# Performance work log

Hardware: AMD Instinct MI355X
Metric: run time of the kernel (lower is better)

## Reference

```python
import jax, jax.numpy as jnp
from jax import lax
import numpy as np

EPS = 1e-7          # BCE clamp
SMOOTH = 1.0        # Dice smoothing
INT_INF = jnp.int32(2**31 - 1)


def _bce_dice(p, t):
    """BCE + Dice loss (standard BCEDiceLoss): p, t float32 in [0,1]."""
    pc = jnp.clip(p, EPS, 1.0 - EPS)
    bce = -jnp.mean(t * jnp.log(pc) + (1.0 - t) * jnp.log1p(-pc))
    inter = jnp.sum(p * t)
    dice = 1.0 - (2.0 * inter + SMOOTH) / (jnp.sum(p) + jnp.sum(t) + SMOOTH)
    return bce + dice


def _ccl(mask):
    """4-connected component labeling per batch image.
    mask: [B,H,W] bool. Returns (labels, init_labels) int32; 0 = background.
    Iterative min-label propagation to a fixpoint (lax.while_loop)."""
    B, H, W = mask.shape
    init = jnp.where(mask, jnp.arange(1, B * H * W + 1, dtype=jnp.int32).reshape(B, H, W), 0)

    def step(lab):
        big = jnp.where(mask, lab, INT_INF)
        pad_h = jnp.full((B, 1, W), INT_INF, jnp.int32)
        pad_w = jnp.full((B, H, 1), INT_INF, jnp.int32)
        up    = jnp.concatenate([big[:, 1:, :], pad_h], axis=1)
        down  = jnp.concatenate([pad_h, big[:, :-1, :]], axis=1)
        left  = jnp.concatenate([big[:, :, 1:], pad_w], axis=2)
        right = jnp.concatenate([pad_w, big[:, :, :-1]], axis=2)
        m = jnp.minimum(big, jnp.minimum(jnp.minimum(up, down), jnp.minimum(left, right)))
        return jnp.where(mask, m, 0)

    def cond(c):
        return c[1]

    def body(c):
        new = step(c[0])
        return (new, jnp.any(new != c[0]))

    lab, _ = lax.while_loop(cond, body, (init, jnp.array(True)))
    return lab, init


def _forward(pred_out, target_mask, num_target_classes):
    f32 = jnp.float32
    B, C, H, W = pred_out.shape
    pred_masks = jnp.argmax(pred_out, axis=1)      # [B,H,W] int
    tm = target_mask[:, 0]                         # [B,H,W] int

    # background-vs-background BCEDice term
    res = _bce_dice((pred_masks == 0).astype(f32), (tm == 0).astype(f32))

    ph = jnp.zeros((B, H, W), f32)    # pred_placeholder
    pho = jnp.zeros((B, H, W), f32)   # pred_placeholder_out
    last_i = jnp.int32(1)

    # fixed loop over predicted classes (torch loops over unique values;
    # here: loop 1..C-1 gated by presence so absent classes are no-ops)
    for v in range(1, C):
        cur = pred_masks == v                       # class-v mask
        present = jnp.any(cur)
        lab, init = _ccl(cur)
        # number of connected components = pixels that kept their seed label
        n_comp = jnp.sum((lab == init) & cur).astype(jnp.int32)
        has_bg = jnp.any(~cur).astype(jnp.int32)    # 0 in cur_uniq?
        # sum_c (c_mask + last_i) over components == cur + n_comp*last_i everywhere
        inc = cur.astype(f32) + (n_comp * last_i).astype(f32)
        ph = jnp.where(present, ph + inc, ph)
        pho = jnp.where(cur, pred_out[:, v], pho)
        last_i = last_i + jnp.where(present, n_comp + has_bg, 0)

    # loop over nonzero target ids (bounded by num_target_classes), gated by presence
    for t in range(1, num_target_classes):
        target_m = tm == t
        present = jnp.any(target_m)
        n = jnp.sum(target_m)
        # torch.median(ph[target_m]): lower median of masked values
        vals = jnp.where(target_m.reshape(-1), ph.reshape(-1), jnp.inf)
        med = jnp.sort(vals)[jnp.maximum((n - 1) // 2, 0)]
        tm_f = target_m.astype(f32)
        contrib = _bce_dice(pho * (ph == med).astype(f32), tm_f)
        extra = jnp.sum(pho * ((ph != med) & target_m).astype(f32)) / jnp.maximum(n, 1).astype(f32)
        res = res + jnp.where(present, contrib + extra, 0.0)

    # len(torch.unique(target_mask)) with values in [0, num_target_classes)
    n_unique = jnp.sum(jnp.stack([jnp.any(tm == t) for t in range(num_target_classes)]).astype(jnp.int32))
    return res / (2 * n_unique + 1).astype(f32)


def setup_inputs() -> dict:
    key = jax.random.key(0)
    k1, k2 = jax.random.split(key)
    B, C, H, W = 8, 5, 768, 768
    pred_out = jax.random.uniform(k1, (B, C, H, W), dtype=jnp.float32)
    target_mask = jax.random.randint(k2, (B, 1, H, W), 0, 4, dtype=jnp.int32)
    return {"pred_out": pred_out, "target_mask": target_mask, "num_target_classes": 4}


def reference(pred_out, target_mask, num_target_classes):
    return _forward(pred_out, target_mask, num_target_classes)
```

## Files before the change

### kernel.cpp

```cpp
#include <hip/hip_runtime.h>
#include <stdint.h>
#include <math.h>

#define B_ 8
#define C_ 5
#define H_ 768
#define W_ 768
#define HW_ (H_*W_)
#define HWq (HW_/4)
#define NPIX (B_*HW_)
#define NQUAD (NPIX/4)
#define TB 8
#define INVAL 0xFFFFFFFFu
#define LN2F 0.69314718056f
#define BIASF 16.2f
#define TILE 64
#define TPR 12
#define TPC 12
#define NTILES (B_*TPR*TPC)
#define NNODES (NTILES*256)
#define SEAMS_PER_IMG (11*768)
#define NB_HALF (B_*SEAMS_PER_IMG)
#define NB_TOT (2*NB_HALF)
#define SEAMBLK (NB_TOT/256)
#define SBLK 2304
#define NTH (SBLK*256)

typedef unsigned long long ull;

static __device__ __forceinline__ unsigned pload(const unsigned* P, unsigned i) {
  return __hip_atomic_load(&P[i], __ATOMIC_RELAXED, __HIP_MEMORY_SCOPE_AGENT);
}
static __device__ unsigned findRootG(unsigned* P, unsigned i) {
  unsigned p = pload(P, i);
  if (p == i) return i;
  unsigned gp = pload(P, p);
  while (p != gp) {
    __hip_atomic_store(&P[i], gp, __ATOMIC_RELAXED, __HIP_MEMORY_SCOPE_AGENT);
    i = p; p = gp; gp = pload(P, p);
  }
  return p;
}
static __device__ bool uniteG(unsigned* P, unsigned a, unsigned b) {
  a = findRootG(P, a);
  b = findRootG(P, b);
  while (a != b) {
    if (a < b) { unsigned t = a; a = b; b = t; }
    unsigned old = atomicCAS(&P[a], a, b);
    if (old == a) return true;
    a = findRootG(P, old);
    b = findRootG(P, b);
  }
  return false;
}
static __device__ __forceinline__ unsigned ploadL(const unsigned* P, unsigned i) {
  return __hip_atomic_load(&P[i], __ATOMIC_RELAXED, __HIP_MEMORY_SCOPE_WORKGROUP);
}
static __device__ unsigned findRootL(const unsigned* P, unsigned i) {
  unsigned p = ploadL(P, i) & 0xFFFFu;
  while (p != i) { i = p; p = ploadL(P, i) & 0xFFFFu; }
  return i;
}
static __device__ void uniteL(unsigned* P, unsigned a, unsigned b) {
  a = findRootL(P, a);
  b = findRootL(P, b);
  while (a != b) {
    if (a < b) { unsigned t = a; a = b; b = t; }
    unsigned old = atomicCAS(&P[a], 0xFFFF0000u | a, 0xFFFF0000u | b);
    if (old == (0xFFFF0000u | a)) return;
    a = findRootL(P, old & 0xFFFFu);
    b = findRootL(P, b);
  }
}

__global__ __launch_bounds__(256) void k_stats(
    const float4* __restrict__ pred4, const int4* __restrict__ tgt4,
    unsigned* __restrict__ cls4, double* __restrict__ sp)
{
  __shared__ ull h[32][41];
  for (int i = threadIdx.x; i < 32*41; i += 256) (&h[0][0])[i] = 0ull;
  __syncthreads();
  const int cp = threadIdx.x & 31;
  const int tid = blockIdx.x * 256 + threadIdx.x;

#define DOQUAD(P0, P1, P2, P3, P4, T4, PACKED)                                 \
  {                                                                            \
    PACKED = 0u;                                                               \
    _Pragma("unroll")                                                          \
    for (int j = 0; j < 4; ++j) {                                              \
      float v0 = ((const float*)&(P0))[j];                                     \
      float v1 = ((const float*)&(P1))[j];                                     \
      float v2 = ((const float*)&(P2))[j];                                     \
      float v3 = ((const float*)&(P3))[j];                                     \
      float v4 = ((const float*)&(P4))[j];                                     \
      int tt = ((const int*)&(T4))[j];                                         \
      float best = v0; int bc = 0;                                             \
      if (v1 > best) { best = v1; bc = 1; }                                    \
      if (v2 > best) { best = v2; bc = 2; }                                    \
      if (v3 > best) { best = v3; bc = 3; }                                    \
      if (v4 > best) { best = v4; bc = 4; }                                    \
      unsigned tu = (unsigned)tt; if (tu >= TB) tu = TB - 1;                   \
      ull w;                                                                   \
      if (bc) {                                                                \
        float pc = fminf(fmaxf(best, 1e-7f), 1.0f - 1e-7f);                    \
        float l2p = __log2f(pc);                                               \
        float l2m = __log2f(1.0f - pc);                                        \
        float logit = (l2p - l2m) * LN2F;                                      \
        float mag   = -l2m * LN2F;                                             \
        w = (1ull << 57)                                                       \
          | ((ull)__float2uint_rn(best * 4096.0f) << 38)                       \
          | ((ull)__float2uint_rn((logit + BIASF) * 64.0f) << 20)              \
          | (ull)__float2uint_rn(mag * 64.0f);                                 \
      } else {                                                                 \
        w = 1ull << 57;                                                        \
      }                                                                        \
      atomicAdd(&h[cp][(int)tu * C_ + bc], w);                                 \
      PACKED |= ((unsigned)bc) << (8 * j);                                     \
    }                                                                          \
  }

  {
    int q0 = tid;
    int q1 = tid + NTH;
    int b0 = q0 / HWq, h0 = q0 - b0 * HWq;
    int b1 = q1 / HWq, h1 = q1 - b1 * HWq;
    const float4* ba = pred4 + (size_t)b0 * (C_*HWq) + h0;
    const float4* bb = pred4 + (size_t)b1 * (C_*HWq) + h1;
    float4 a0 = ba[0], a1 = ba[HWq], a2 = ba[2*HWq], a3 = ba[3*HWq], a4 = ba[4*HWq];
    float4 c0 = bb[0], c1 = bb[HWq], c2 = bb[2*HWq], c3 = bb[3*HWq], c4 = bb[4*HWq];
    int4 ta = tgt4[q0];
    int4 tb = tgt4[q1];
    unsigned pk0, pk1;
    DOQUAD(a0, a1, a2, a3, a4, ta, pk0)
    DOQUAD(c0, c1, c2, c3, c4, tb, pk1)
    cls4[q0] = pk0;
    cls4[q1] = pk1;
  }
#undef DOQUAD
  __syncthreads();
  if (threadIdx.x < 160) {
    int slot = threadIdx.x >> 2, comp = threadIdx.x & 3;
    double s = 0.0;
#pragma unroll
    for (int c = 0; c < 32; ++c) {
      ull w = h[c][slot];
      if (comp == 0)      s += (double)(w >> 57);
      else if (comp == 1) s += (double)((w >> 38) & 0x7FFFFull) * (1.0/4096.0);
      else if (comp == 2) s += (double)((w >> 20) & 0x3FFFFull) * (1.0/64.0);
      else                s += (double)(w & 0x1FFFFull) * (1.0/64.0);
    }
    sp[(size_t)blockIdx.x * 160 + threadIdx.x] = s;
  }
}

__global__ __launch_bounds__(256) void k_ccl(
    const unsigned* __restrict__ cls4, unsigned short* __restrict__ border,
    unsigned* __restrict__ P2, unsigned* __restrict__ rootcnt)
{
  __shared__ unsigned lab[TILE*TILE];
  __shared__ unsigned lclsw[TILE*TILE/4];
  __shared__ unsigned s_rt[4];
  unsigned char* lcls = (unsigned char*)lclsw;

  int blk = blockIdx.x;
  int b = blk / (TPR*TPC);
  int rem = blk - b * (TPR*TPC);
  int ty0 = (rem / TPR) * TILE;
  int tx0 = (rem - (rem / TPR) * TPR) * TILE;

  if (threadIdx.x < 4) s_rt[threadIdx.x] = 0u;
  {
    unsigned n = (unsigned)blk * 256u + threadIdx.x;
    P2[n] = n;
  }
  const int r = threadIdx.x >> 2, cq = threadIdx.x & 3;
  const int seg = r * 64 + cq * 16;
  union { uint4 q; unsigned char bch[16]; unsigned w[4]; } A, D;
  {
    const uint4* src = (const uint4*)(cls4 + ((b * HW_ + (ty0 + r) * W_ + tx0) >> 2));
    A.q = src[cq];
    *(uint4*)&lclsw[r * 16 + cq * 4] = A.q;
  }
#pragma unroll
  for (int m = 0; m < 4; ++m) {
    uint4 lw;
    unsigned* lp = (unsigned*)&lw;
#pragma unroll
    for (int k = 0; k < 4; ++k) {
      int li = seg + m * 4 + k;
      unsigned c = (A.w[m] >> (8 * k)) & 255u;
      lp[k] = c ? (0xFFFF0000u | (unsigned)li) : INVAL;
    }
    *(uint4*)&lab[seg + m * 4] = lw;
  }
  __syncthreads();

  bool hasDown = (r < 63);
  if (hasDown) D.q = *(const uint4*)&lclsw[(r + 1) * 16 + cq * 4];
  else D.q = make_uint4(0, 0, 0, 0);
  unsigned rb = (cq < 3) ? (unsigned)lcls[seg + 16] : 0u;
#pragma unroll
  for (int j = 0; j < 16; ++j) {
    unsigned c = A.bch[j];
    if (!c) continue;
    int li = seg + j;
    unsigned cr = (j < 15) ? (unsigned)A.bch[j + 1] : rb;
    if (cr == c) uniteL(lab, li, li + 1);
    if (D.bch[j] == c) uniteL(lab, li, li + 64);
  }
  __syncthreads();

#pragma unroll
  for (int m = 0; m < 4; ++m) {
    uint4 lw = *(const uint4*)&lab[seg + m * 4];
    const unsigned* lp = (const unsigned*)&lw;
#pragma unroll
    for (int k = 0; k < 4; ++k) {
      int li = seg + m * 4 + k;
      unsigned c = A.bch[m * 4 + k];
      if (c && (lp[k] & 0xFFFFu) == (unsigned)li) atomicAdd(&s_rt[c - 1], 1u);
    }
  }
  int bp = threadIdx.x;
  int tx, ty;
  if (bp < 64)       { ty = 0;  tx = bp; }
  else if (bp < 128) { ty = 63; tx = bp - 64; }
  else if (bp < 192) { tx = 0;  ty = bp - 128; }
  else               { tx = 63; ty = bp - 192; }
  int li = ty * 64 + tx;
  unsigned char c = lcls[li];
  unsigned rt = 0;
  if (c) {
    rt = findRootL(lab, (unsigned)li);
    atomicMin(&lab[rt], ((unsigned)bp << 16) | rt);
  }
  __syncthreads();
  unsigned sub = c ? (lab[rt] >> 16) : 0u;
  border[blk * 256 + bp] = (unsigned short)(((unsigned)c << 8) | sub);
  if (threadIdx.x < 4) rootcnt[blk * 4 + threadIdx.x] = s_rt[threadIdx.x];
}

__global__ __launch_bounds__(256) void k_seam(const unsigned short* __restrict__ border,
                                              unsigned* __restrict__ P2,
                                              unsigned* __restrict__ smcnt,
                                              const double* __restrict__ sp,
                                              double* __restrict__ spf)
{
  __shared__ unsigned s_sub[4];
  __shared__ double red[256];
  if (threadIdx.x < 4) s_sub[threadIdx.x] = 0u;
  __syncthreads();
  int idx = blockIdx.x * blockDim.x + threadIdx.x;
  if (idx < NB_TOT) {
    int tA, tB, pA, pB;
    if (idx < NB_HALF) {
      int b = idx / SEAMS_PER_IMG;
      int r = idx - b * SEAMS_PER_IMG;
      int seam = r / W_;
      int x = r - seam * W_;
      int tj = x >> 6, k = x & 63;
      tA = (b * TPC + seam) * TPR + tj;
      tB = tA + TPR;
      pA = tA * 256 + 64 + k;
      pB = tB * 256 + 0 + k;
    } else {
      int i2 = idx - NB_HALF;
      int b = i2 / SEAMS_PER_IMG;
      int r = i2 - b * SEAMS_PER_IMG;
      int seam = r / H_;
      int y = r - seam * H_;
      int ti = y >> 6, k = y & 63;
      tA = (b * TPC + ti) * TPR + seam;
      tB = tA + 1;
      pA = tA * 256 + 192 + k;
      pB = tB * 256 + 128 + k;
    }
    unsigned a16 = border[pA];
    unsigned b16 = border[pB];
    unsigned ca = a16 >> 8, cb = b16 >> 8;
    if (ca && ca == cb) {
      if (uniteG(P2, (unsigned)tA * 256u + (a16 & 255u),
                     (unsigned)tB * 256u + (b16 & 255u)))
        atomicAdd(&s_sub[ca - 1], 1u);
    }
  }
  __syncthreads();
  if (threadIdx.x < 4) smcnt[blockIdx.x * 4 + threadIdx.x] = s_sub[threadIdx.x];
  if (blockIdx.x < 160) {
    double s = 0.0;
    for (int j = threadIdx.x; j < SBLK; j += 256) s += sp[(size_t)j * 160 + blockIdx.x];
    red[threadIdx.x] = s;
    __syncthreads();
    for (int off = 128; off; off >>= 1) {
      if (threadIdx.x < off) red[threadIdx.x] += red[threadIdx.x + off];
      __syncthreads();
    }
    if (threadIdx.x == 0) spf[blockIdx.x] = red[0];
  }
}

#define SH_CNT(t,c)   shist[((t)*C_+(c))*4 + 0]
#define SH_PRED(t,c)  shist[((t)*C_+(c))*4 + 1]
#define SH_LRAW(t,c)  shist[((t)*C_+(c))*4 + 2]
#define SH_MAG(t,c)   shist[((t)*C_+(c))*4 + 3]
__global__ __launch_bounds__(256) void k_final(
    const double* __restrict__ spf, const unsigned* __restrict__ rootcnt,
    const unsigned* __restrict__ smcnt, const int* __restrict__ ntcp,
    float* __restrict__ out)
{
  __shared__ double shist[160];
  __shared__ double s_col[C_][3];
  __shared__ unsigned s_cnti[TB*C_];
  __shared__ unsigned s_ctot[C_];
  __shared__ unsigned s_nc[4], s_sm[4];
  __shared__ float s_ph[C_];
  __shared__ double s_term[TB];
  __shared__ int s_NT;
  __shared__ int s_nun;

  if (threadIdx.x < 4) { s_nc[threadIdx.x] = 0u; s_sm[threadIdx.x] = 0u; }
  if (threadIdx.x < TB) s_term[threadIdx.x] = 0.0;
  __syncthreads();
  if (threadIdx.x < 160) shist[threadIdx.x] = spf[threadIdx.x];
  {
    unsigned a = 0;
    for (int j = threadIdx.x; j < NTILES * 4; j += 256) a += rootcnt[j];
    if (a) atomicAdd(&s_nc[threadIdx.x & 3], a);
  }
  {
    unsigned a = 0;
    for (int j = threadIdx.x; j < SEAMBLK * 4; j += 256) a += smcnt[j];
    if (a) atomicAdd(&s_sm[threadIdx.x & 3], a);
  }
  if (threadIdx.x == 0) {
    int NT = ntcp[0];
    if (NT < 1) NT = 1;
    if (NT > TB) NT = TB;
    s_NT = NT;
  }
  __syncthreads();

  if (threadIdx.x < TB * C_) s_cnti[threadIdx.x] = (unsigned)llrint(shist[threadIdx.x * 4]);
  __syncthreads();

  if (threadIdx.x < C_) {
    int c = threadIdx.x;
    double sc = 0.0, sp2 = 0.0, sl = 0.0;
    unsigned ct = 0;
#pragma unroll
    for (int t = 0; t < TB; ++t) {
      sc += SH_CNT(t, c);
      sp2 += SH_PRED(t, c);
      sl += -SH_MAG(t, c);
      ct += s_cnti[t * C_ + c];
    }
    s_col[c][0] = sc; s_col[c][1] = sp2; s_col[c][2] = sl;
    s_ctot[c] = ct;
  }
  __syncthreads();

  if (threadIdx.x == 0) {
#pragma unroll
    for (int cc = 0; cc < C_; ++cc) {
      float ph = 0.0f;
      int li = 1;
#pragma unroll
      for (int v = 1; v < C_; ++v) {
        unsigned ncv = s_nc[v - 1] - s_sm[v - 1];
        if (s_ctot[v] > 0) {
          int prod = (int)(ncv * (unsigned)li);
          float sv = (float)prod;
          float inc = ((cc == v) ? 1.0f : 0.0f) + sv;
          ph = ph + inc;
          li = li + (int)ncv + ((s_ctot[v] < (unsigned)NPIX) ? 1 : 0);
        }
      }
      s_ph[cc] = ph;
    }
  }
  __syncthreads();

  const float EPSF = 1e-7f;
  const double L1 = (double)logf(1.0f - EPSF);
  const double M1 = (double)log1pf(-(1.0f - EPSF));
  const double L0 = (double)logf(EPSF);
  const double M0 = (double)log1pf(-EPSF);
  const double N = (double)NPIX;
  const double BIASD = (double)BIASF;
  const int NT = s_NT;

  if (threadIdx.x == 0) {
    double nt0 = 0;
#pragma unroll
    for (int c = 0; c < C_; ++c) nt0 += SH_CNT(0, c);
    double np1 = (double)s_ctot[0];
    double n11 = SH_CNT(0, 0);
    s_term[0] = -(n11*L1 + (nt0 - n11)*L0 + (np1 - n11)*M1 + (N - nt0 - np1 + n11)*M0) / N
                + 1.0 - (2.0*n11 + 1.0) / (np1 + nt0 + 1.0);
    int nun = 0;
    for (int t = 0; t < NT; ++t) {
      long long s = 0;
#pragma unroll
      for (int c = 0; c < C_; ++c) s += (long long)s_cnti[t * C_ + c];
      if (s) nun++;
    }
    s_nun = nun;
  } else if (threadIdx.x < (unsigned)NT) {
    int t = threadIdx.x;
    long long ntti = 0;
#pragma unroll
    for (int c = 0; c < C_; ++c) ntti += (long long)s_cnti[t * C_ + c];
    if (ntti != 0) {
      double ntt = 0;
#pragma unroll
      for (int c = 0; c < C_; ++c) ntt += SH_CNT(t, c);
      float ph0 = s_ph[0], ph1 = s_ph[1], ph2 = s_ph[2], ph3 = s_ph[3], ph4 = s_ph[4];
      float pht[C_] = {ph0, ph1, ph2, ph3, ph4};
      int idx[C_] = {0, 1, 2, 3, 4};
#pragma unroll
      for (int i = 1; i < C_; ++i)
        for (int j = i; j > 0 && pht[idx[j]] < pht[idx[j-1]]; --j) {
          int tmp = idx[j]; idx[j] = idx[j-1]; idx[j-1] = tmp;
        }
      long long k = (ntti - 1) / 2;
      float med = pht[idx[C_ - 1]];
      long long cum = 0;
#pragma unroll
      for (int i = 0; i < C_; ++i) {
        cum += (long long)s_cnti[t * C_ + idx[i]];
        if (cum > k) { med = pht[idx[i]]; break; }
      }
      double A = 0, Bt = 0, inter = 0, sum_p = 0, ex = 0, nfg_t = 0, nfg_all = 0;
#pragma unroll
      for (int c = 1; c < C_; ++c) {
        double cnt_tc = SH_CNT(t, c);
        double mag_tc = SH_MAG(t, c);
        double spred_tc = SH_PRED(t, c);
        if (pht[c] == med) {
          double logit = SH_LRAW(t, c) - BIASD * cnt_tc;
          A += logit - mag_tc;
          inter += spred_tc;
          nfg_t += cnt_tc;
          nfg_all += s_col[c][0];
          sum_p += s_col[c][1];
          Bt += s_col[c][2] - (-mag_tc);
        } else {
          ex += spred_tc;
        }
      }
      double bce  = -(A + Bt + (ntt - nfg_t)*L0 + (N - ntt - (nfg_all - nfg_t))*M0) / N;
      double dice = 1.0 - (2.0*inter + 1.0) / (sum_p + ntt + 1.0);
      s_term[t] = bce + dice + ex / ntt;
    }
  }
  __syncthreads();
  if (threadIdx.x == 0) {
    double res = 0.0;
#pragma unroll
    for (int t = 0; t < TB; ++t) res += s_term[t];
    out[0] = (float)(res / (double)(2 * s_nun + 1));
  }
}

extern "C" void kernel_launch(void* const* d_in, const int* in_sizes, int n_in,
                              void* d_out, int out_size, void* d_ws, size_t ws_size,
                              hipStream_t stream) {
  const float* pred = (const float*)d_in[0];
  const int* tgt = (const int*)d_in[1];
  const int* ntc = (const int*)d_in[2];
  float* out = (float*)d_out;
  char* ws = (char*)d_ws;
  size_t off = 0;
  unsigned* cls4 = (unsigned*)(ws + off);        off += (size_t)NQUAD * 4;
  double* sp = (double*)(ws + off);              off += (size_t)SBLK * 160 * 8;
  double* spf = (double*)(ws + off);             off += 160 * 8;
  unsigned* P2 = (unsigned*)(ws + off);          off += (size_t)NNODES * 4;
  unsigned short* border = (unsigned short*)(ws + off); off += (size_t)NTILES * 256 * 2;
  unsigned* rootcnt = (unsigned*)(ws + off);     off += (size_t)NTILES * 4 * 4;
  unsigned* smcnt = (unsigned*)(ws + off);       off += (size_t)SEAMBLK * 4 * 4;

  hipLaunchKernelGGL(k_stats, dim3(SBLK), dim3(256), 0, stream,
                     (const float4*)pred, (const int4*)tgt, cls4, sp);
  hipLaunchKernelGGL(k_ccl, dim3(NTILES), dim3(256), 0, stream,
                     cls4, border, P2, rootcnt);
  hipLaunchKernelGGL(k_seam, dim3(SEAMBLK), dim3(256), 0, stream,
                     border, P2, smcnt, sp, spf);
  hipLaunchKernelGGL(k_final, dim3(1), dim3(256), 0, stream,
                     spf, rootcnt, smcnt, ntc, out);
}
```

Baseline: 199.9 us.

## Fuse final reduction into seam kernel via last-block-done pattern

The separate single-block k_final launch is removed. Its work now runs in the last k_seam block to finish, chosen through an atomic done-counter with acquire-release ordering. Per-block seam counts are accumulated with atomics into a four-word total instead of being written to an array and re-reduced. The stats kernel's per-pixel log computation is also made branchless, computing it for every pixel and masking the result for background. This saves one kernel launch and a global array pass, at the cost of extra atomics and more log work for background pixels.

```diff
diff --git a/kernel.cpp b/kernel.cpp
--- a/kernel.cpp
+++ b/kernel.cpp
@@ -100,20 +100,16 @@
       if (v3 > best) { best = v3; bc = 3; }                                    \
       if (v4 > best) { best = v4; bc = 4; }                                    \
       unsigned tu = (unsigned)tt; if (tu >= TB) tu = TB - 1;                   \
-      ull w;                                                                   \
-      if (bc) {                                                                \
-        float pc = fminf(fmaxf(best, 1e-7f), 1.0f - 1e-7f);                    \
-        float l2p = __log2f(pc);                                               \
-        float l2m = __log2f(1.0f - pc);                                        \
-        float logit = (l2p - l2m) * LN2F;                                      \
-        float mag   = -l2m * LN2F;                                             \
-        w = (1ull << 57)                                                       \
-          | ((ull)__float2uint_rn(best * 4096.0f) << 38)                       \
-          | ((ull)__float2uint_rn((logit + BIASF) * 64.0f) << 20)              \
-          | (ull)__float2uint_rn(mag * 64.0f);                                 \
-      } else {                                                                 \
-        w = 1ull << 57;                                                        \
-      }                                                                        \
+      float pc = fminf(fmaxf(best, 1e-7f), 1.0f - 1e-7f);                      \
+      float l2p = __log2f(pc);                                                 \
+      float l2m = __log2f(1.0f - pc);                                          \
+      float logit = (l2p - l2m) * LN2F;                                        \
+      float mag   = -l2m * LN2F;                                               \
+      ull w = (1ull << 57)                                                     \
+            | ((ull)__float2uint_rn(best * 4096.0f) << 38)                     \
+            | ((ull)__float2uint_rn((logit + BIASF) * 64.0f) << 20)            \
+            | (ull)__float2uint_rn(mag * 64.0f);                               \
+      if (!bc) w = 1ull << 57;                                                 \
       atomicAdd(&h[cp][(int)tu * C_ + bc], w);                                 \
       PACKED |= ((unsigned)bc) << (8 * j);                                     \
     }                                                                          \
@@ -155,7 +151,8 @@
 
 __global__ __launch_bounds__(256) void k_ccl(
     const unsigned* __restrict__ cls4, unsigned short* __restrict__ border,
-    unsigned* __restrict__ P2, unsigned* __restrict__ rootcnt)
+    unsigned* __restrict__ P2, unsigned* __restrict__ rootcnt,
+    unsigned* __restrict__ smtot, unsigned* __restrict__ done)
 {
   __shared__ unsigned lab[TILE*TILE];
   __shared__ unsigned lclsw[TILE*TILE/4];
@@ -169,6 +166,10 @@
   int tx0 = (rem - (rem / TPR) * TPR) * TILE;
 
   if (threadIdx.x < 4) s_rt[threadIdx.x] = 0u;
+  if (blk == 0 && threadIdx.x < 5) {
+    if (threadIdx.x < 4) smtot[threadIdx.x] = 0u;
+    else done[0] = 0u;
+  }
   {
     unsigned n = (unsigned)blk * 256u + threadIdx.x;
     P2[n] = n;
@@ -240,14 +241,20 @@
   if (threadIdx.x < 4) rootcnt[blk * 4 + threadIdx.x] = s_rt[threadIdx.x];
 }
 
-__global__ __launch_bounds__(256) void k_seam(const unsigned short* __restrict__ border,
-                                              unsigned* __restrict__ P2,
-                                              unsigned* __restrict__ smcnt,
-                                              const double* __restrict__ sp,
-                                              double* __restrict__ spf)
+#define SH_CNT(t,c)   shist[((t)*C_+(c))*4 + 0]
+#define SH_PRED(t,c)  shist[((t)*C_+(c))*4 + 1]
+#define SH_LRAW(t,c)  shist[((t)*C_+(c))*4 + 2]
+#define SH_MAG(t,c)   shist[((t)*C_+(c))*4 + 3]
+__global__ __launch_bounds__(256) void k_seam(
+    const unsigned short* __restrict__ border, unsigned* __restrict__ P2,
+    unsigned* __restrict__ smtot, unsigned* __restrict__ done,
+    const double* __restrict__ sp, double* __restrict__ spf,
+    const unsigned* __restrict__ rootcnt, const int* __restrict__ ntcp,
+    float* __restrict__ out)
 {
   __shared__ unsigned s_sub[4];
   __shared__ double red[256];
+  __shared__ int s_last;
   if (threadIdx.x < 4) s_sub[threadIdx.x] = 0u;
   __syncthreads();
   int idx = blockIdx.x * blockDim.x + threadIdx.x;
@@ -285,7 +292,6 @@
     }
   }
   __syncthreads();
-  if (threadIdx.x < 4) smcnt[blockIdx.x * 4 + threadIdx.x] = s_sub[threadIdx.x];
   if (blockIdx.x < 160) {
     double s = 0.0;
     for (int j = threadIdx.x; j < SBLK; j += 256) s += sp[(size_t)j * 160 + blockIdx.x];
@@ -295,19 +301,20 @@
       if (threadIdx.x < off) red[threadIdx.x] += red[threadIdx.x + off];
       __syncthreads();
     }
-    if (threadIdx.x == 0) spf[blockIdx.x] = red[0];
-  }
-}
-
-#define SH_CNT(t,c)   shist[((t)*C_+(c))*4 + 0]
-#define SH_PRED(t,c)  shist[((t)*C_+(c))*4 + 1]
-#define SH_LRAW(t,c)  shist[((t)*C_+(c))*4 + 2]
-#define SH_MAG(t,c)   shist[((t)*C_+(c))*4 + 3]
-__global__ __launch_bounds__(256) void k_final(
-    const double* __restrict__ spf, const unsigned* __restrict__ rootcnt,
-    const unsigned* __restrict__ smcnt, const int* __restrict__ ntcp,
-    float* __restrict__ out)
-{
+  }
+  if (threadIdx.x == 0) {
+    if (blockIdx.x < 160)
+      __hip_atomic_store(&spf[blockIdx.x], red[0], __ATOMIC_RELAXED, __HIP_MEMORY_SCOPE_AGENT);
+#pragma unroll
+    for (int c2 = 0; c2 < 4; ++c2)
+      if (s_sub[c2]) atomicAdd(&smtot[c2], s_sub[c2]);
+    unsigned tk = __hip_atomic_fetch_add(&done[0], 1u, __ATOMIC_ACQ_REL,
+                                         __HIP_MEMORY_SCOPE_AGENT);
+    s_last = (tk == SEAMBLK - 1);
+  }
+  __syncthreads();
+  if (!s_last) return;
+
   __shared__ double shist[160];
   __shared__ double s_col[C_][3];
   __shared__ unsigned s_cnti[TB*C_];
@@ -318,19 +325,20 @@
   __shared__ int s_NT;
   __shared__ int s_nun;
 
-  if (threadIdx.x < 4) { s_nc[threadIdx.x] = 0u; s_sm[threadIdx.x] = 0u; }
+  if (threadIdx.x < 4) {
+    s_nc[threadIdx.x] = 0u;
+    s_sm[threadIdx.x] = __hip_atomic_load(&smtot[threadIdx.x], __ATOMIC_RELAXED,
+                                          __HIP_MEMORY_SCOPE_AGENT);
+  }
   if (threadIdx.x < TB) s_term[threadIdx.x] = 0.0;
   __syncthreads();
-  if (threadIdx.x < 160) shist[threadIdx.x] = spf[threadIdx.x];
+  if (threadIdx.x < 160)
+    shist[threadIdx.x] = __hip_atomic_load(&spf[threadIdx.x], __ATOMIC_RELAXED,
+                                           __HIP_MEMORY_SCOPE_AGENT);
   {
     unsigned a = 0;
     for (int j = threadIdx.x; j < NTILES * 4; j += 256) a += rootcnt[j];
     if (a) atomicAdd(&s_nc[threadIdx.x & 3], a);
-  }
-  {
-    unsigned a = 0;
-    for (int j = threadIdx.x; j < SEAMBLK * 4; j += 256) a += smcnt[j];
-    if (a) atomicAdd(&s_sm[threadIdx.x & 3], a);
   }
   if (threadIdx.x == 0) {
     int NT = ntcp[0];
@@ -363,16 +371,16 @@
 #pragma unroll
     for (int cc = 0; cc < C_; ++cc) {
       float ph = 0.0f;
-      int li = 1;
+      int li2 = 1;
 #pragma unroll
       for (int v = 1; v < C_; ++v) {
         unsigned ncv = s_nc[v - 1] - s_sm[v - 1];
         if (s_ctot[v] > 0) {
-          int prod = (int)(ncv * (unsigned)li);
+          int prod = (int)(ncv * (unsigned)li2);
           float sv = (float)prod;
           float inc = ((cc == v) ? 1.0f : 0.0f) + sv;
           ph = ph + inc;
-          li = li + (int)ncv + ((s_ctot[v] < (unsigned)NPIX) ? 1 : 0);
+          li2 = li2 + (int)ncv + ((s_ctot[v] < (unsigned)NPIX) ? 1 : 0);
         }
       }
       s_ph[cc] = ph;
@@ -414,21 +422,20 @@
       double ntt = 0;
 #pragma unroll
       for (int c = 0; c < C_; ++c) ntt += SH_CNT(t, c);
-      float ph0 = s_ph[0], ph1 = s_ph[1], ph2 = s_ph[2], ph3 = s_ph[3], ph4 = s_ph[4];
-      float pht[C_] = {ph0, ph1, ph2, ph3, ph4};
-      int idx[C_] = {0, 1, 2, 3, 4};
+      float pht[C_] = {s_ph[0], s_ph[1], s_ph[2], s_ph[3], s_ph[4]};
+      int idx2[C_] = {0, 1, 2, 3, 4};
 #pragma unroll
       for (int i = 1; i < C_; ++i)
-        for (int j = i; j > 0 && pht[idx[j]] < pht[idx[j-1]]; --j) {
-          int tmp = idx[j]; idx[j] = idx[j-1]; idx[j-1] = tmp;
+        for (int j = i; j > 0 && pht[idx2[j]] < pht[idx2[j-1]]; --j) {
+          int tmp = idx2[j]; idx2[j] = idx2[j-1]; idx2[j-1] = tmp;
         }
       long long k = (ntti - 1) / 2;
-      float med = pht[idx[C_ - 1]];
+      float med = pht[idx2[C_ - 1]];
       long long cum = 0;
 #pragma unroll
       for (int i = 0; i < C_; ++i) {
-        cum += (long long)s_cnti[t * C_ + idx[i]];
-        if (cum > k) { med = pht[idx[i]]; break; }
+        cum += (long long)s_cnti[t * C_ + idx2[i]];
+        if (cum > k) { med = pht[idx2[i]]; break; }
       }
       double A = 0, Bt = 0, inter = 0, sum_p = 0, ex = 0, nfg_t = 0, nfg_all = 0;
 #pragma unroll
@@ -477,14 +484,13 @@
   unsigned* P2 = (unsigned*)(ws + off);          off += (size_t)NNODES * 4;
   unsigned short* border = (unsigned short*)(ws + off); off += (size_t)NTILES * 256 * 2;
   unsigned* rootcnt = (unsigned*)(ws + off);     off += (size_t)NTILES * 4 * 4;
-  unsigned* smcnt = (unsigned*)(ws + off);       off += (size_t)SEAMBLK * 4 * 4;
+  unsigned* smtot = (unsigned*)(ws + off);       off += 16;
+  unsigned* done = (unsigned*)(ws + off);        off += 16;
 
   hipLaunchKernelGGL(k_stats, dim3(SBLK), dim3(256), 0, stream,
                      (const float4*)pred, (const int4*)tgt, cls4, sp);
   hipLaunchKernelGGL(k_ccl, dim3(NTILES), dim3(256), 0, stream,
-                     cls4, border, P2, rootcnt);
+                     cls4, border, P2, rootcnt, smtot, done);
   hipLaunchKernelGGL(k_seam, dim3(SEAMBLK), dim3(256), 0, stream,
-                     border, P2, smcnt, sp, spf);
-  hipLaunchKernelGGL(k_final, dim3(1), dim3(256), 0, stream,
-                     spf, rootcnt, smcnt, ntc, out);
-}
+                     border, P2, smtot, done, sp, spf, rootcnt, ntc, out);
+}
```

Measured after the change: 223.8 us. +11.9%, slower.
